# Optimization experiments

Hardware: AMD Instinct MI355X
Metric: run time of the kernel (lower is better)

The kernel has to match this reference:

```python
import jax, jax.numpy as jnp
import numpy as np

WS = 8          # window size
N = WS * WS     # tokens per window
H = 4           # num heads
DIM = 128
HD = DIM // H   # head dim
SCALE = HD ** -0.5


def _rel_pos_index(ws):
    coords = np.stack(np.meshgrid(np.arange(ws), np.arange(ws), indexing='ij')).reshape(2, -1)
    rel = coords[:, :, None] - coords[:, None, :]          # [2, N, N]
    rel = rel.transpose(1, 2, 0)                           # [N, N, 2]
    rel[..., 0] += ws - 1
    rel[..., 1] += ws - 1
    rel[..., 0] *= 2 * ws - 1
    return jnp.asarray(rel.sum(-1), dtype=jnp.int32)       # [N, N]

_REL_IDX = _rel_pos_index(WS)


def setup_inputs() -> dict:
    key = jax.random.key(0)
    ks = jax.random.split(key, 7)
    B_ = 8192
    nW = 64
    return {
        'x': jax.random.normal(ks[0], (B_, N, DIM), dtype=jnp.float32),
        'mask': jax.random.normal(ks[1], (nW, N, N), dtype=jnp.float32),
        'qkv_w': jax.random.normal(ks[2], (3 * DIM, DIM), dtype=jnp.float32) * 0.02,
        'qkv_b': jax.random.normal(ks[3], (3 * DIM,), dtype=jnp.float32) * 0.02,
        'proj_w': jax.random.normal(ks[4], (DIM, DIM), dtype=jnp.float32) * 0.02,
        'proj_b': jax.random.normal(ks[5], (DIM,), dtype=jnp.float32) * 0.02,
        'rel_pos_bias': jax.random.normal(ks[6], ((2 * WS - 1) ** 2, H), dtype=jnp.float32) * 0.02,
    }


def reference(x, mask, qkv_w, qkv_b, proj_w, proj_b, rel_pos_bias):
    B_, n, c = x.shape
    nW = mask.shape[0]
    qkv = x @ qkv_w.T + qkv_b                               # [B_, N, 3C]
    qkv = qkv.reshape(B_, n, 3, H, HD).transpose(2, 0, 3, 1, 4)
    q, k, v = qkv[0], qkv[1], qkv[2]                        # [B_, H, N, HD]
    attn = jnp.einsum('bhnd,bhmd->bhnm', q * SCALE, k)      # [B_, H, N, N]
    bias = rel_pos_bias[_REL_IDX.reshape(-1)].reshape(n, n, H)
    attn = attn + bias.transpose(2, 0, 1)[None]
    attn = attn.reshape(B_ // nW, nW, H, n, n) + mask[None, :, None, :, :]
    attn = attn.reshape(B_, H, n, n)
    attn = jax.nn.softmax(attn, axis=-1)
    out = jnp.einsum('bhnm,bhmd->bnhd', attn, v).reshape(B_, n, c)
    return out @ proj_w.T + proj_b
```

## Files before the change

kernel.cpp:

```cpp
#include <hip/hip_runtime.h>
#include <stdint.h>

typedef __attribute__((ext_vector_type(8))) short short8;
typedef __attribute__((ext_vector_type(4))) short s16x4;
typedef __attribute__((ext_vector_type(4))) float f32x4;
typedef __attribute__((ext_vector_type(4))) uint32_t u32x4;
typedef __attribute__((ext_vector_type(2))) uint32_t u32x2;

#define LOG2E   1.4426950408889634f
#define SCALE_Q 0.17677669529663687f

__device__ __forceinline__ uint16_t f2bf(float f) {
    uint32_t u = __builtin_bit_cast(uint32_t, f);
    u += 0x7FFFu + ((u >> 16) & 1u);
    return (uint16_t)(u >> 16);
}

__device__ __forceinline__ uint32_t cvtpk(float a, float b) {
    uint32_t r;
    asm("v_cvt_pk_bf16_f32 %0, %1, %2" : "=v"(r) : "v"(a), "v"(b));
    return r;
}

__global__ void prep_kernel(const float* __restrict__ qkv_w, const float* __restrict__ qkv_b,
                            const float* __restrict__ proj_w, const float* __restrict__ rel_b,
                            uint16_t* __restrict__ wq, float* __restrict__ bq,
                            uint16_t* __restrict__ wp, float* __restrict__ bTs) {
    int t = blockIdx.x * 256 + threadIdx.x;
    if (t < 384 * 128) {
        int o = t >> 7;
        float s = (o < 128) ? SCALE_Q * LOG2E : 1.0f;
        wq[t] = f2bf(qkv_w[t] * s);
    }
    if (t < 384) bq[t] = qkv_b[t] * ((t < 128) ? SCALE_Q * LOG2E : 1.0f);
    if (t < 128 * 128) wp[t] = f2bf(proj_w[t]);
    if (t < 4 * 64 * 64) {
        int h = t & 3, nm = t >> 2, n = nm >> 6, m = nm & 63;
        int idx = ((n >> 3) - (m >> 3) + 7) * 15 + ((n & 7) - (m & 7) + 7);
        bTs[(h * 64 + n) * 64 + m] = rel_b[idx * 4 + h] * LOG2E;
    }
}

__global__ __launch_bounds__(256, 3) void winattn_kernel(
    const float* __restrict__ x, const float* __restrict__ mask,
    const uint16_t* __restrict__ wq, const float* __restrict__ bq,
    const uint16_t* __restrict__ wp, const float* __restrict__ pb,
    const float* __restrict__ bTs, float* __restrict__ out)
{
    __shared__ uint16_t S1[16896];
    __shared__ uint16_t Vt[9216];

    const int b    = blockIdx.x;
    const int w    = b & 63;
    const int wid  = threadIdx.x >> 6;
    const int lane = threadIdx.x & 63;
    const int l15  = lane & 15;
    const int lg   = lane >> 4;

    short8 xa[4][4];
    const float* xb = x + (size_t)b * 8192;
    #pragma unroll
    for (int tt = 0; tt < 4; ++tt) {
      #pragma unroll
      for (int ks = 0; ks < 4; ++ks) {
        const float* p = xb + (tt*16 + l15)*128 + ks*32 + lg*8;
        f32x4 f0 = *(const f32x4*)p;
        f32x4 f1 = *(const f32x4*)(p + 4);
        u32x4 u = { cvtpk(f0[0],f0[1]), cvtpk(f0[2],f0[3]),
                    cvtpk(f1[0],f1[1]), cvtpk(f1[2],f1[3]) };
        xa[tt][ks] = __builtin_bit_cast(short8, u);
      }
    }
    #pragma unroll
    for (int ct = 0; ct < 6; ++ct) {
        const int tile = wid + 4*ct;
        short8 wb[4];
        #pragma unroll
        for (int ks = 0; ks < 4; ++ks)
            wb[ks] = *(const short8*)(wq + (tile*16 + l15)*128 + ks*32 + lg*8);
        f32x4 bqv = *(const f32x4*)(bq + tile*16 + lg*4);
        #pragma unroll
        for (int tt = 0; tt < 4; ++tt) {
            f32x4 acc = {0.f,0.f,0.f,0.f};
            #pragma unroll
            for (int ks = 0; ks < 4; ++ks)
                acc = __builtin_amdgcn_mfma_f32_16x16x32_bf16(wb[ks], xa[tt][ks], acc, 0,0,0);
            const int token = tt*16 + l15;
            if (ct < 4) {
                u32x2 wv = { cvtpk(acc[0]+bqv[0], acc[1]+bqv[1]),
                             cvtpk(acc[2]+bqv[2], acc[3]+bqv[3]) };
                *(u32x2*)&S1[token*264 + tile*16 + lg*4] = wv;
            } else {
                const int vd0 = tile*16 + lg*4 - 256;
                #pragma unroll
                for (int r = 0; r < 4; ++r)
                    Vt[(vd0 + r)*72 + token] = (uint16_t)cvtpk(acc[r]+bqv[r], acc[r]+bqv[r]);
            }
        }
    }
    __syncthreads();

    const int h = wid;
    short8 kf[4], qf[4];
    #pragma unroll
    for (int mt = 0; mt < 4; ++mt)
        kf[mt] = *(const short8*)&S1[(mt*16 + l15)*264 + 128 + h*32 + lg*8];
    #pragma unroll
    for (int nt = 0; nt < 4; ++nt)
        qf[nt] = *(const short8*)&S1[(nt*16 + l15)*264 + h*32 + lg*8];
    __syncthreads();

    f32x4 sacc[4][4];
    #pragma unroll
    for (int mt = 0; mt < 4; ++mt) {
      #pragma unroll
      for (int nt = 0; nt < 4; ++nt) {
        f32x4 z = {0.f,0.f,0.f,0.f};
        sacc[mt][nt] = __builtin_amdgcn_mfma_f32_16x16x32_bf16(kf[mt], qf[nt], z, 0,0,0);
      }
    }

    const float* bTh = bTs + h*4096;
    const float* mkw = mask + w*4096;
    float rcpv[4];
    #pragma unroll
    for (int nt = 0; nt < 4; ++nt) {
        const int off = (nt*16 + l15)*64 + lg*4;
        float mx = -3.0e38f;
        #pragma unroll
        for (int mt = 0; mt < 4; ++mt) {
            f32x4 bb = *(const f32x4*)(bTh + off + mt*16);
            f32x4 mm = *(const f32x4*)(mkw + off + mt*16);
            #pragma unroll
            for (int r = 0; r < 4; ++r) {
                float t = fmaf(mm[r], LOG2E, sacc[mt][nt][r] + bb[r]);
                sacc[mt][nt][r] = t;
                mx = fmaxf(mx, t);
            }
        }
        mx = fmaxf(mx, __shfl_xor(mx, 16));
        mx = fmaxf(mx, __shfl_xor(mx, 32));
        float sum = 0.f;
        #pragma unroll
        for (int mt = 0; mt < 4; ++mt) {
          #pragma unroll
          for (int r = 0; r < 4; ++r) {
            float p = exp2f(sacc[mt][nt][r] - mx);
            sacc[mt][nt][r] = p;
            sum += p;
          }
        }
        sum += __shfl_xor(sum, 16);
        sum += __shfl_xor(sum, 32);
        rcpv[nt] = __builtin_amdgcn_rcpf(sum);
    }

    short8 pa[4][2];
    #pragma unroll
    for (int nt = 0; nt < 4; ++nt) {
      #pragma unroll
      for (int a = 0; a < 2; ++a) {
        u32x4 u = { cvtpk(sacc[2*a][nt][0],   sacc[2*a][nt][1]),
                    cvtpk(sacc[2*a][nt][2],   sacc[2*a][nt][3]),
                    cvtpk(sacc[2*a+1][nt][0], sacc[2*a+1][nt][1]),
                    cvtpk(sacc[2*a+1][nt][2], sacc[2*a+1][nt][3]) };
        pa[nt][a] = __builtin_bit_cast(short8, u);
      }
    }

    f32x4 oacc[2][4];
    #pragma unroll
    for (int dt = 0; dt < 2; ++dt) {
        const uint16_t* vrow = Vt + (h*32 + dt*16 + l15)*72;
        short8 va[2];
        #pragma unroll
        for (int a = 0; a < 2; ++a) {
            s16x4 x0 = *(const s16x4*)(vrow + a*32 + lg*4);
            s16x4 x1 = *(const s16x4*)(vrow + a*32 + 16 + lg*4);
            va[a] = __builtin_shufflevector(x0, x1, 0,1,2,3,4,5,6,7);
        }
        #pragma unroll
        for (int nt = 0; nt < 4; ++nt) {
            f32x4 acc = {0.f,0.f,0.f,0.f};
            acc = __builtin_amdgcn_mfma_f32_16x16x32_bf16(va[0], pa[nt][0], acc, 0,0,0);
            acc = __builtin_amdgcn_mfma_f32_16x16x32_bf16(va[1], pa[nt][1], acc, 0,0,0);
            oacc[dt][nt] = acc;
        }
    }

    #pragma unroll
    for (int dt = 0; dt < 2; ++dt) {
      #pragma unroll
      for (int nt = 0; nt < 4; ++nt) {
        const float rc = rcpv[nt];
        f32x4 o = oacc[dt][nt];
        u32x2 wv = { cvtpk(o[0]*rc, o[1]*rc), cvtpk(o[2]*rc, o[3]*rc) };
        *(u32x2*)&S1[(nt*16 + l15)*136 + h*32 + dt*16 + lg*4] = wv;
      }
    }
    __syncthreads();

    short8 of[4][4];
    #pragma unroll
    for (int rt = 0; rt < 4; ++rt)
      #pragma unroll
      for (int ks = 0; ks < 4; ++ks)
        of[rt][ks] = *(const short8*)&S1[(rt*16 + l15)*136 + ks*32 + lg*8];

    float* outb = out + (size_t)b * 8192;
    #pragma unroll
    for (int ct = 0; ct < 2; ++ct) {
        const int cbase = wid*32 + ct*16;
        short8 wf[4];
        #pragma unroll
        for (int ks = 0; ks < 4; ++ks)
            wf[ks] = *(const short8*)(wp + (cbase + l15)*128 + ks*32 + lg*8);
        const float pbias = pb[cbase + l15];
        #pragma unroll
        for (int rt = 0; rt < 4; ++rt) {
            f32x4 acc = {0.f,0.f,0.f,0.f};
            #pragma unroll
            for (int ks = 0; ks < 4; ++ks)
                acc = __builtin_amdgcn_mfma_f32_16x16x32_bf16(of[rt][ks], wf[ks], acc, 0,0,0);
            #pragma unroll
            for (int r = 0; r < 4; ++r)
                outb[(rt*16 + lg*4 + r)*128 + cbase + l15] = acc[r] + pbias;
        }
    }
}

extern "C" void kernel_launch(void* const* d_in, const int* in_sizes, int n_in,
                              void* d_out, int out_size, void* d_ws, size_t ws_size,
                              hipStream_t stream) {
    const float* x      = (const float*)d_in[0];
    const float* mask   = (const float*)d_in[1];
    const float* qkv_w  = (const float*)d_in[2];
    const float* qkv_b  = (const float*)d_in[3];
    const float* proj_w = (const float*)d_in[4];
    const float* proj_b = (const float*)d_in[5];
    const float* rel_b  = (const float*)d_in[6];
    float* out = (float*)d_out;

    char* ws = (char*)d_ws;
    uint16_t* wq  = (uint16_t*)ws;
    float*    bq  = (float*)(ws + 98304);
    uint16_t* wp  = (uint16_t*)(ws + 99840);
    float*    bTs = (float*)(ws + 132608);

    const int B_ = in_sizes[0] / (64 * 128);

    hipLaunchKernelGGL(prep_kernel, dim3(192), dim3(256), 0, stream,
                       qkv_w, qkv_b, proj_w, rel_b, wq, bq, wp, bTs);
    hipLaunchKernelGGL(winattn_kernel, dim3(B_), dim3(256), 0, stream,
                       x, mask, wq, bq, wp, proj_b, bTs, out);
}
```

Baseline: 386.2 us.

## Defer V projection past softmax and alias LDS to fit four blocks per CU

The V part of the QKV projection moves after the score and softmax phase. x is reloaded from global memory and reconverted to bf16 for it, and the V tile and the attention-output staging buffer now alias into a single smaller shared buffer. This cuts LDS use from about 52KB to 36KB and shortens register live ranges, so launch bounds rise from 3 to 4 blocks per CU. In exchange, x is read from global twice per block and one more barrier is added.

Result: slower. 541.0 us (+40.1%).

```diff
diff --git a/kernel.cpp b/kernel.cpp
--- a/kernel.cpp
+++ b/kernel.cpp
@@ -41,14 +41,17 @@
     }
 }
 
-__global__ __launch_bounds__(256, 3) void winattn_kernel(
+__global__ __launch_bounds__(256, 4) void winattn_kernel(
     const float* __restrict__ x, const float* __restrict__ mask,
     const uint16_t* __restrict__ wq, const float* __restrict__ bq,
     const uint16_t* __restrict__ wp, const float* __restrict__ pb,
     const float* __restrict__ bTs, float* __restrict__ out)
 {
-    __shared__ uint16_t S1[16896];
-    __shared__ uint16_t Vt[9216];
+    __shared__ uint16_t SCR[18432];
+
+    uint16_t* S1 = SCR;
+    uint16_t* Vt = SCR;
+    uint16_t* Os = SCR + 9216;
 
     const int b    = blockIdx.x;
     const int w    = b & 63;
@@ -57,44 +60,39 @@
     const int l15  = lane & 15;
     const int lg   = lane >> 4;
 
-    short8 xa[4][4];
     const float* xb = x + (size_t)b * 8192;
-    #pragma unroll
-    for (int tt = 0; tt < 4; ++tt) {
-      #pragma unroll
-      for (int ks = 0; ks < 4; ++ks) {
-        const float* p = xb + (tt*16 + l15)*128 + ks*32 + lg*8;
-        f32x4 f0 = *(const f32x4*)p;
-        f32x4 f1 = *(const f32x4*)(p + 4);
-        u32x4 u = { cvtpk(f0[0],f0[1]), cvtpk(f0[2],f0[3]),
-                    cvtpk(f1[0],f1[1]), cvtpk(f1[2],f1[3]) };
-        xa[tt][ks] = __builtin_bit_cast(short8, u);
-      }
-    }
-    #pragma unroll
-    for (int ct = 0; ct < 6; ++ct) {
-        const int tile = wid + 4*ct;
-        short8 wb[4];
-        #pragma unroll
-        for (int ks = 0; ks < 4; ++ks)
-            wb[ks] = *(const short8*)(wq + (tile*16 + l15)*128 + ks*32 + lg*8);
-        f32x4 bqv = *(const f32x4*)(bq + tile*16 + lg*4);
+    {
+        short8 xa[4][4];
         #pragma unroll
         for (int tt = 0; tt < 4; ++tt) {
-            f32x4 acc = {0.f,0.f,0.f,0.f};
+          #pragma unroll
+          for (int ks = 0; ks < 4; ++ks) {
+            const float* p = xb + (tt*16 + l15)*128 + ks*32 + lg*8;
+            f32x4 f0 = *(const f32x4*)p;
+            f32x4 f1 = *(const f32x4*)(p + 4);
+            u32x4 u = { cvtpk(f0[0],f0[1]), cvtpk(f0[2],f0[3]),
+                        cvtpk(f1[0],f1[1]), cvtpk(f1[2],f1[3]) };
+            xa[tt][ks] = __builtin_bit_cast(short8, u);
+          }
+        }
+        #pragma unroll
+        for (int ct = 0; ct < 4; ++ct) {
+            const int tile = wid + 4*ct;
+            short8 wb[4];
             #pragma unroll
             for (int ks = 0; ks < 4; ++ks)
-                acc = __builtin_amdgcn_mfma_f32_16x16x32_bf16(wb[ks], xa[tt][ks], acc, 0,0,0);
-            const int token = tt*16 + l15;
-            if (ct < 4) {
+                wb[ks] = *(const short8*)(wq + (tile*16 + l15)*128 + ks*32 + lg*8);
+            f32x4 bqv = *(const f32x4*)(bq + tile*16 + lg*4);
+            #pragma unroll
+            for (int tt = 0; tt < 4; ++tt) {
+                f32x4 acc = {0.f,0.f,0.f,0.f};
+                #pragma unroll
+                for (int ks = 0; ks < 4; ++ks)
+                    acc = __builtin_amdgcn_mfma_f32_16x16x32_bf16(wb[ks], xa[tt][ks], acc, 0,0,0);
+                const int token = tt*16 + l15;
                 u32x2 wv = { cvtpk(acc[0]+bqv[0], acc[1]+bqv[1]),
                              cvtpk(acc[2]+bqv[2], acc[3]+bqv[3]) };
                 *(u32x2*)&S1[token*264 + tile*16 + lg*4] = wv;
-            } else {
-                const int vd0 = tile*16 + lg*4 - 256;
-                #pragma unroll
-                for (int r = 0; r < 4; ++r)
-                    Vt[(vd0 + r)*72 + token] = (uint16_t)cvtpk(acc[r]+bqv[r], acc[r]+bqv[r]);
             }
         }
     }
@@ -168,6 +166,44 @@
       }
     }
 
+    {
+        short8 xa2[4][4];
+        #pragma unroll
+        for (int tt = 0; tt < 4; ++tt) {
+          #pragma unroll
+          for (int ks = 0; ks < 4; ++ks) {
+            const float* p = xb + (tt*16 + l15)*128 + ks*32 + lg*8;
+            f32x4 f0 = *(const f32x4*)p;
+            f32x4 f1 = *(const f32x4*)(p + 4);
+            u32x4 u = { cvtpk(f0[0],f0[1]), cvtpk(f0[2],f0[3]),
+                        cvtpk(f1[0],f1[1]), cvtpk(f1[2],f1[3]) };
+            xa2[tt][ks] = __builtin_bit_cast(short8, u);
+          }
+        }
+        #pragma unroll
+        for (int ct = 4; ct < 6; ++ct) {
+            const int tile = wid + 4*ct;
+            short8 wb[4];
+            #pragma unroll
+            for (int ks = 0; ks < 4; ++ks)
+                wb[ks] = *(const short8*)(wq + (tile*16 + l15)*128 + ks*32 + lg*8);
+            f32x4 bqv = *(const f32x4*)(bq + tile*16 + lg*4);
+            #pragma unroll
+            for (int tt = 0; tt < 4; ++tt) {
+                f32x4 acc = {0.f,0.f,0.f,0.f};
+                #pragma unroll
+                for (int ks = 0; ks < 4; ++ks)
+                    acc = __builtin_amdgcn_mfma_f32_16x16x32_bf16(wb[ks], xa2[tt][ks], acc, 0,0,0);
+                const int token = tt*16 + l15;
+                const int vd0 = tile*16 + lg*4 - 256;
+                #pragma unroll
+                for (int r = 0; r < 4; ++r)
+                    Vt[(vd0 + r)*72 + token] = (uint16_t)cvtpk(acc[r]+bqv[r], acc[r]+bqv[r]);
+            }
+        }
+    }
+    __syncthreads();
+
     f32x4 oacc[2][4];
     #pragma unroll
     for (int dt = 0; dt < 2; ++dt) {
@@ -187,7 +223,6 @@
             oacc[dt][nt] = acc;
         }
     }
-
     #pragma unroll
     for (int dt = 0; dt < 2; ++dt) {
       #pragma unroll
@@ -195,7 +230,7 @@
         const float rc = rcpv[nt];
         f32x4 o = oacc[dt][nt];
         u32x2 wv = { cvtpk(o[0]*rc, o[1]*rc), cvtpk(o[2]*rc, o[3]*rc) };
-        *(u32x2*)&S1[(nt*16 + l15)*136 + h*32 + dt*16 + lg*4] = wv;
+        *(u32x2*)&Os[(nt*16 + l15)*136 + h*32 + dt*16 + lg*4] = wv;
       }
     }
     __syncthreads();
@@ -205,7 +240,7 @@
     for (int rt = 0; rt < 4; ++rt)
       #pragma unroll
       for (int ks = 0; ks < 4; ++ks)
-        of[rt][ks] = *(const short8*)&S1[(rt*16 + l15)*136 + ks*32 + lg*8];
+        of[rt][ks] = *(const short8*)&Os[(rt*16 + l15)*136 + ks*32 + lg*8];
 
     float* outb = out + (size_t)b * 8192;
     #pragma unroll
```
